# Performance work log

Hardware: AMD Instinct MI355X
Metric: run time of the kernel (lower is better)

## Reference

```python
import jax, jax.numpy as jnp
import numpy as np

B, T, C, H = 16, 2048, 1024, 64  # batch, seq (== block_size), n_embd, head_size


def setup_inputs() -> dict:
    key = jax.random.key(0)
    ks = jax.random.split(key, 4)
    s = 1.0 / np.sqrt(C)  # Linear default init scale
    return {
        "x": jax.random.normal(ks[0], (B, T, C), dtype=jnp.float32),
        "Wq": jax.random.normal(ks[1], (C, H), dtype=jnp.float32) * s,
        "bq": jnp.zeros((H,), dtype=jnp.float32),
        "Wk": jax.random.normal(ks[2], (C, H), dtype=jnp.float32) * s,
        "bk": jnp.zeros((H,), dtype=jnp.float32),
        "Wv": jax.random.normal(ks[3], (C, H), dtype=jnp.float32) * s,
        "bv": jnp.zeros((H,), dtype=jnp.float32),
    }


def reference(x, Wq, bq, Wk, bk, Wv, bv):
    # q, k, v: (B, T, H)
    q = x @ Wq + bq
    k = x @ Wk + bk
    v = x @ Wv + bv
    # scores (B, T, T); NOTE: original code has NO 1/sqrt(H) scaling
    wei = jnp.einsum("btd,bsd->bts", q, k)
    t = x.shape[1]
    causal = jnp.tril(jnp.ones((t, t), dtype=bool))
    wei = jnp.where(causal, wei, -jnp.inf)
    # NOTE: original code applies softmax over dim=1 (query axis), kept faithfully
    wei = jax.nn.softmax(wei, axis=1)
    # dropout is identity at p=0 / eval
    out = jnp.einsum("bts,bsd->btd", wei, v)  # (B, T, H)
    return out
```

## Files before the change

### kernel.cpp

```cpp
#include <hip/hip_runtime.h>
#include <hip/hip_bf16.h>
#include <math.h>

#define TT 2048
#define NB 16

typedef short short8 __attribute__((ext_vector_type(8)));
typedef float f32x4 __attribute__((ext_vector_type(4)));
typedef unsigned short us4 __attribute__((ext_vector_type(4)));

#define MFMA16(a,b,c) __builtin_amdgcn_mfma_f32_16x16x32_bf16((a),(b),(c),0,0,0)

typedef const __attribute__((address_space(1))) unsigned gas_u32;
typedef __attribute__((address_space(3))) unsigned las_u32;

__device__ __forceinline__ void gll16(const void* g, void* l) {
    __builtin_amdgcn_global_load_lds((gas_u32*)g, (las_u32*)l, 16, 0, 0);
}

__device__ __forceinline__ unsigned short bf16rn(float f) {
    unsigned u = __float_as_uint(f);
    u += 0x7FFFu + ((u >> 16) & 1u);
    return (unsigned short)(u >> 16);
}
__device__ __forceinline__ float bf16tof(unsigned short h) {
    return __uint_as_float(((unsigned)h) << 16);
}

__global__ void wprep_kernel(const float* __restrict__ Wq,
                             const float* __restrict__ Wk,
                             const float* __restrict__ Wv,
                             short* __restrict__ WT)
{
    const int m = blockIdx.x >> 6, n = blockIdx.x & 63, tid = threadIdx.x;
    const float* W = (m == 0) ? Wq : ((m == 1) ? Wk : Wv);
    const float sc = (m == 0) ? 1.4426950408889634f : 1.f;
    const int k0 = tid * 4;
    us4 hv, lv;
#pragma unroll
    for (int r = 0; r < 4; ++r) {
        float v = W[(size_t)(k0 + r) * 64 + n] * sc;
        unsigned short hh = bf16rn(v);
        hv[r] = hh;
        lv[r] = bf16rn(v - bf16tof(hh));
    }
    *(us4*)&WT[((size_t)(m * 2 + 0) * 64 + n) * 1024 + k0] = hv;
    *(us4*)&WT[((size_t)(m * 2 + 1) * 64 + n) * 1024 + k0] = lv;
}

__global__ __launch_bounds__(256, 2) void qkv_kernel(
    const float* __restrict__ x,
    const float* __restrict__ bq, const float* __restrict__ bk,
    const float* __restrict__ bv,
    const short* __restrict__ WT,
    short* __restrict__ qhl, short* __restrict__ khl, short* __restrict__ vT)
{
    __shared__ short xs[16384];
    __shared__ short ws[24576];
    const int tid = threadIdx.x;
    const int w = tid >> 6, l15 = tid & 15, g = (tid >> 4) & 3;
    const int t0 = blockIdx.x * 128;

    f32x4 acc[12][2];
    const f32x4 z = {0.f, 0.f, 0.f, 0.f};
#pragma unroll
    for (int i = 0; i < 12; ++i) { acc[i][0] = z; acc[i][1] = z; }

#pragma unroll 1
    for (int kc = 0; kc < 16; ++kc) {
#pragma unroll
        for (int p = 0; p < 12; ++p) {
            int u = tid + p * 256;
            int part = u / 1536; int r = u - part * 1536;
            int kk = r / 768;    int r2 = r - kk * 768;
            int n = r2 >> 2, g8 = r2 & 3;
            int m = n >> 6, nn = n & 63;
            const short* src = WT + (((size_t)((m * 2 + part) * 64 + nn)) << 10)
                                  + kc * 64 + kk * 32 + g8 * 8;
            gll16(src, &ws[((tid & ~63) + p * 256) * 8]);
        }
#pragma unroll
        for (int p = 0; p < 4; ++p) {
            int idx = tid + p * 256;
            int kk = idx >> 9; int rem = idx & 511;
            int row = rem >> 2, g8 = rem & 3;
            const float* xp = x + (size_t)(t0 + row) * 1024 + kc * 64 + kk * 32 + g8 * 8;
            f32x4 a = *(const f32x4*)xp;
            f32x4 b2 = *(const f32x4*)(xp + 4);
            short8 h8, l8;
#pragma unroll
            for (int j = 0; j < 4; ++j) {
                unsigned short hh = bf16rn(a[j]);
                h8[j] = (short)hh; l8[j] = (short)bf16rn(a[j] - bf16tof(hh));
                hh = bf16rn(b2[j]);
                h8[j + 4] = (short)hh; l8[j + 4] = (short)bf16rn(b2[j] - bf16tof(hh));
            }
            *(short8*)&xs[((kk * 128 + row) * 4 + g8) * 8] = h8;
            *(short8*)&xs[(((2 + kk) * 128 + row) * 4 + g8) * 8] = l8;
        }
        __syncthreads();

#pragma unroll
        for (int kk = 0; kk < 2; ++kk) {
            short8 xf[2][2];
#pragma unroll
            for (int m2 = 0; m2 < 2; ++m2)
#pragma unroll
                for (int part = 0; part < 2; ++part)
                    xf[m2][part] = *(const short8*)
                        &xs[(((part * 2 + kk) * 128 + (w * 32 + m2 * 16 + l15)) * 4 + g) * 8];
#pragma unroll
            for (int Nb = 0; Nb < 12; ++Nb) {
                short8 wh = *(const short8*)&ws[(((kk) * 192 + Nb * 16 + l15) * 4 + g) * 8];
                short8 wl = *(const short8*)&ws[(((2 + kk) * 192 + Nb * 16 + l15) * 4 + g) * 8];
#pragma unroll
                for (int m2 = 0; m2 < 2; ++m2) {
                    if (Nb < 8) {
                        acc[Nb][m2] = MFMA16(wh, xf[m2][0], acc[Nb][m2]);
                        acc[Nb][m2] = MFMA16(wh, xf[m2][1], acc[Nb][m2]);
                        acc[Nb][m2] = MFMA16(wl, xf[m2][0], acc[Nb][m2]);
                    } else {
                        acc[Nb][m2] = MFMA16(xf[m2][0], wh, acc[Nb][m2]);
                        acc[Nb][m2] = MFMA16(xf[m2][1], wh, acc[Nb][m2]);
                        acc[Nb][m2] = MFMA16(xf[m2][0], wl, acc[Nb][m2]);
                    }
                }
            }
        }
        __syncthreads();
    }

    const float LOG2E = 1.4426950408889634f;
#pragma unroll
    for (int Nb = 0; Nb < 12; ++Nb) {
#pragma unroll
        for (int m2 = 0; m2 < 2; ++m2) {
            f32x4 a = acc[Nb][m2];
            if (Nb < 8) {
                const bool isq = (Nb < 4);
                const int nbase = (Nb & 3) * 16 + g * 4;
                const int trow = t0 + w * 32 + m2 * 16 + l15;
                const float* bias = isq ? bq : bk;
                us4 hv, lv;
#pragma unroll
                for (int r = 0; r < 4; ++r) {
                    float v = a[r] + (isq ? bias[nbase + r] * LOG2E : bias[nbase + r]);
                    unsigned short hh = bf16rn(v);
                    hv[r] = hh; lv[r] = bf16rn(v - bf16tof(hh));
                }
                short* dst = (isq ? qhl : khl) + ((size_t)trow * 2) * 64 + nbase;
                *(us4*)dst = hv;
                *(us4*)(dst + 64) = lv;
            } else {
                const int d = (Nb - 8) * 16 + l15;
                const int tbase = t0 + w * 32 + m2 * 16 + g * 4;
                const float bvd = bv[d];
                us4 pk;
#pragma unroll
                for (int r = 0; r < 4; ++r) pk[r] = bf16rn(a[r] + bvd);
                const int b = tbase >> 11, ttl = tbase & 2047;
                *(us4*)&vT[((size_t)(b * 64 + d)) * 2048 + ttl] = pk;
            }
        }
    }
}

__global__ __launch_bounds__(256, 2) void colstats_kernel(
    const short* __restrict__ qhl, const short* __restrict__ khl,
    float* __restrict__ ccol)
{
    __shared__ short kb[8192];
    __shared__ short qb[8192];
    const int tid = threadIdx.x;
    const int w = tid >> 6, l15 = tid & 15, g = (tid >> 4) & 3;
    const int sblk = blockIdx.x, b = blockIdx.y;
    const int s0 = sblk * 64;

#pragma unroll
    for (int p = 0; p < 4; ++p) {
        int u = tid + p * 256;
        int part = u >> 9, kk = (u >> 8) & 1, row = (u >> 2) & 63, g8 = u & 3;
        const short* src = khl + ((size_t)(b * TT + s0 + row) * 2 + part) * 64
                               + kk * 32 + g8 * 8;
        gll16(src, &kb[((tid & ~63) + p * 256) * 8]);
    }

    short8 kf[2][2];
    float m_slot[4], d_slot[4];
    const f32x4 z = {0.f, 0.f, 0.f, 0.f};

#pragma unroll 1
    for (int tt = sblk; tt < 32; ++tt) {
#pragma unroll
        for (int p = 0; p < 4; ++p) {
            int u = tid + p * 256;
            int part = u >> 9, kk = (u >> 8) & 1, row = (u >> 2) & 63, g8 = u & 3;
            const short* src = qhl + ((size_t)(b * TT + tt * 64 + row) * 2 + part) * 64
                                   + kk * 32 + g8 * 8;
            gll16(src, &qb[((tid & ~63) + p * 256) * 8]);
        }
        __syncthreads();
        if (tt == sblk) {
#pragma unroll
            for (int kk = 0; kk < 2; ++kk)
#pragma unroll
                for (int part = 0; part < 2; ++part)
                    kf[kk][part] = *(const short8*)
                        &kb[(((part * 2 + kk) * 64 + w * 16 + l15) * 4 + g) * 8];
        }
        f32x4 a4[4];
#pragma unroll
        for (int tb = 0; tb < 4; ++tb) {
            a4[tb] = z;
#pragma unroll
            for (int kk = 0; kk < 2; ++kk) {
                short8 qh = *(const short8*)&qb[(((kk) * 64 + tb * 16 + l15) * 4 + g) * 8];
                short8 ql = *(const short8*)&qb[(((2 + kk) * 64 + tb * 16 + l15) * 4 + g) * 8];
                a4[tb] = MFMA16(kf[kk][0], qh, a4[tb]);
                a4[tb] = MFMA16(kf[kk][0], ql, a4[tb]);
                a4[tb] = MFMA16(kf[kk][1], qh, a4[tb]);
            }
        }
        if (tt == sblk) {
#pragma unroll
            for (int tb = 0; tb < 4; ++tb)
#pragma unroll
                for (int r = 0; r < 4; ++r)
                    if (tb * 16 + l15 < w * 16 + g * 4 + r) a4[tb][r] = -INFINITY;
#pragma unroll
            for (int r = 0; r < 4; ++r) {
                float mx = fmaxf(fmaxf(a4[0][r], a4[1][r]), fmaxf(a4[2][r], a4[3][r]));
                mx = fmaxf(mx, __shfl_xor(mx, 1));
                mx = fmaxf(mx, __shfl_xor(mx, 2));
                mx = fmaxf(mx, __shfl_xor(mx, 4));
                mx = fmaxf(mx, __shfl_xor(mx, 8));
                m_slot[r] = fmaxf(mx, 0.f);
                d_slot[r] = exp2f(a4[0][r] - m_slot[r]) + exp2f(a4[1][r] - m_slot[r])
                          + exp2f(a4[2][r] - m_slot[r]) + exp2f(a4[3][r] - m_slot[r]);
            }
        } else {
#pragma unroll
            for (int r = 0; r < 4; ++r)
                d_slot[r] += exp2f(a4[0][r] - m_slot[r]) + exp2f(a4[1][r] - m_slot[r])
                           + exp2f(a4[2][r] - m_slot[r]) + exp2f(a4[3][r] - m_slot[r]);
        }
        __syncthreads();
    }
#pragma unroll
    for (int r = 0; r < 4; ++r) {
        float dv = d_slot[r];
        dv += __shfl_xor(dv, 1); dv += __shfl_xor(dv, 2);
        dv += __shfl_xor(dv, 4); dv += __shfl_xor(dv, 8);
        d_slot[r] = dv;
    }
    if (l15 == 0) {
        f32x4 c;
#pragma unroll
        for (int r = 0; r < 4; ++r) c[r] = m_slot[r] + log2f(d_slot[r]);
        *(f32x4*)&ccol[(size_t)b * TT + s0 + w * 16 + g * 4] = c;
    }
}

__global__ __launch_bounds__(256, 2) void attnout_kernel(
    const short* __restrict__ qhl, const short* __restrict__ khl,
    const short* __restrict__ vT, const float* __restrict__ ccol,
    float* __restrict__ out)
{
    __shared__ short kb[8192];
    __shared__ short vb[4096];
    __shared__ short eb[4096];
    __shared__ float cb[64];
    const int tid = threadIdx.x;
    const int w = tid >> 6, l15 = tid & 15, g = (tid >> 4) & 3;
    const int tblk = blockIdx.x, b = blockIdx.y;
    const int t0 = tblk * 64;

    short8 qf[4][2][2];
#pragma unroll
    for (int tb = 0; tb < 4; ++tb)
#pragma unroll
        for (int kk = 0; kk < 2; ++kk)
#pragma unroll
            for (int part = 0; part < 2; ++part)
                qf[tb][kk][part] = *(const short8*)
                    (qhl + ((size_t)(b * TT + t0 + tb * 16 + l15) * 2 + part) * 64
                         + kk * 32 + g * 8);

    f32x4 oacc[4];
    const f32x4 z = {0.f, 0.f, 0.f, 0.f};
#pragma unroll
    for (int tb = 0; tb < 4; ++tb) oacc[tb] = z;

#pragma unroll 1
    for (int ss = 0; ss <= tblk; ++ss) {
        const int s0 = ss * 64;
#pragma unroll
        for (int p = 0; p < 4; ++p) {
            int u = tid + p * 256;
            int part = u >> 9, kk = (u >> 8) & 1, row = (u >> 2) & 63, g8 = u & 3;
            gll16(khl + ((size_t)(b * TT + s0 + row) * 2 + part) * 64 + kk * 32 + g8 * 8,
                  &kb[((tid & ~63) + p * 256) * 8]);
        }
#pragma unroll
        for (int p = 0; p < 2; ++p) {
            int u = tid + p * 256;
            int kgs = u >> 8, d = (u >> 2) & 63, g8 = u & 3;
            gll16(vT + ((size_t)(b * 64 + d)) * 2048 + s0 + kgs * 32 + g8 * 8,
                  &vb[((tid & ~63) + p * 256) * 8]);
        }
        if (tid < 64) cb[tid] = ccol[(size_t)b * TT + s0 + tid];
        __syncthreads();

        short8 kf2[2][2];
#pragma unroll
        for (int kk = 0; kk < 2; ++kk)
#pragma unroll
            for (int part = 0; part < 2; ++part)
                kf2[kk][part] = *(const short8*)
                    &kb[(((part * 2 + kk) * 64 + w * 16 + l15) * 4 + g) * 8];

        f32x4 a4[4];
#pragma unroll
        for (int tb = 0; tb < 4; ++tb) {
            a4[tb] = z;
#pragma unroll
            for (int kk = 0; kk < 2; ++kk) {
                a4[tb] = MFMA16(kf2[kk][0], qf[tb][kk][0], a4[tb]);
                a4[tb] = MFMA16(kf2[kk][0], qf[tb][kk][1], a4[tb]);
                a4[tb] = MFMA16(kf2[kk][1], qf[tb][kk][0], a4[tb]);
            }
        }
        const f32x4 c4 = *(const f32x4*)&cb[w * 16 + g * 4];
        const bool diag = (ss == tblk);
#pragma unroll
        for (int tb = 0; tb < 4; ++tb) {
            us4 pk;
#pragma unroll
            for (int r = 0; r < 4; ++r) {
                float e = exp2f(a4[tb][r] - c4[r]);
                if (diag && (tb * 16 + l15 < w * 16 + g * 4 + r)) e = 0.f;
                pk[r] = bf16rn(e);
            }
            const int kgs = w >> 1, g8s = (w & 1) * 2 + (g >> 1), j0 = (g & 1) * 4;
            *(us4*)&eb[((kgs * 64 + tb * 16 + l15) * 4 + g8s) * 8 + j0] = pk;
        }
        __syncthreads();

        short8 vf[2];
#pragma unroll
        for (int kgs = 0; kgs < 2; ++kgs)
            vf[kgs] = *(const short8*)&vb[(((kgs * 64 + w * 16 + l15) * 4 + g) * 8)];
#pragma unroll
        for (int tb = 0; tb < 4; ++tb)
#pragma unroll
            for (int kgs = 0; kgs < 2; ++kgs) {
                short8 ef = *(const short8*)&eb[(((kgs * 64 + tb * 16 + l15) * 4 + g) * 8)];
                oacc[tb] = MFMA16(vf[kgs], ef, oacc[tb]);
            }
        __syncthreads();
    }
#pragma unroll
    for (int tb = 0; tb < 4; ++tb) {
        const int t = t0 + tb * 16 + l15;
        const int d0 = w * 16 + g * 4;
        *(f32x4*)(out + ((size_t)(b * TT + t)) * 64 + d0) = oacc[tb];
    }
}

extern "C" void kernel_launch(void* const* d_in, const int* in_sizes, int n_in,
                              void* d_out, int out_size, void* d_ws, size_t ws_size,
                              hipStream_t stream)
{
    const float* x  = (const float*)d_in[0];
    const float* Wq = (const float*)d_in[1];
    const float* bq = (const float*)d_in[2];
    const float* Wk = (const float*)d_in[3];
    const float* bk = (const float*)d_in[4];
    const float* Wv = (const float*)d_in[5];
    const float* bv = (const float*)d_in[6];

    char* wsb = (char*)d_ws;
    short* qhl = (short*)wsb;
    short* khl = (short*)(wsb + 8388608);
    short* vTb = (short*)(wsb + 16777216);
    short* WT  = (short*)(wsb + 20971520);
    float* ccol = (float*)(wsb + 21757952);

    wprep_kernel<<<dim3(192), 256, 0, stream>>>(Wq, Wk, Wv, WT);
    qkv_kernel<<<dim3(256), 256, 0, stream>>>(x, bq, bk, bv, WT, qhl, khl, vTb);
    colstats_kernel<<<dim3(32, NB), 256, 0, stream>>>(qhl, khl, ccol);
    attnout_kernel<<<dim3(32, NB), 256, 0, stream>>>(qhl, khl, vTb, ccol, (float*)d_out);
}
```

Baseline: 359.4 us.

## Rebalance causal work across blocks and split column-stats with atomic accumulation

The QKV projection now uses 64-row tiles, doubling the grid, and drops the extra low-part MFMA for V. Column stats are split over query chunks with a fixed-zero max and atomically accumulated sums, with a zeroing kernel added before it. The attention-output kernel pairs a short and a long 32-row query tile per block so each block does similar causal work. Dropping the running max risks overflow in exp2 for large scores, atomics make summation order nondeterministic, and computing V in plain bf16 loses some precision.

```diff
diff --git a/kernel.cpp b/kernel.cpp
--- a/kernel.cpp
+++ b/kernel.cpp
@@ -48,6 +48,10 @@
     *(us4*)&WT[((size_t)(m * 2 + 1) * 64 + n) * 1024 + k0] = lv;
 }
 
+__global__ void zero_kernel(float* __restrict__ p) {
+    p[blockIdx.x * 256 + threadIdx.x] = 0.f;
+}
+
 __global__ __launch_bounds__(256, 2) void qkv_kernel(
     const float* __restrict__ x,
     const float* __restrict__ bq, const float* __restrict__ bk,
@@ -55,16 +59,16 @@
     const short* __restrict__ WT,
     short* __restrict__ qhl, short* __restrict__ khl, short* __restrict__ vT)
 {
-    __shared__ short xs[16384];
+    __shared__ short xs[8192];
     __shared__ short ws[24576];
     const int tid = threadIdx.x;
     const int w = tid >> 6, l15 = tid & 15, g = (tid >> 4) & 3;
-    const int t0 = blockIdx.x * 128;
-
-    f32x4 acc[12][2];
+    const int t0 = blockIdx.x * 64;
+
+    f32x4 acc[12];
     const f32x4 z = {0.f, 0.f, 0.f, 0.f};
 #pragma unroll
-    for (int i = 0; i < 12; ++i) { acc[i][0] = z; acc[i][1] = z; }
+    for (int i = 0; i < 12; ++i) acc[i] = z;
 
 #pragma unroll 1
     for (int kc = 0; kc < 16; ++kc) {
@@ -80,9 +84,9 @@
             gll16(src, &ws[((tid & ~63) + p * 256) * 8]);
         }
 #pragma unroll
-        for (int p = 0; p < 4; ++p) {
+        for (int p = 0; p < 2; ++p) {
             int idx = tid + p * 256;
-            int kk = idx >> 9; int rem = idx & 511;
+            int kk = idx >> 8; int rem = idx & 255;
             int row = rem >> 2, g8 = rem & 3;
             const float* xp = x + (size_t)(t0 + row) * 1024 + kc * 64 + kk * 32 + g8 * 8;
             f32x4 a = *(const f32x4*)xp;
@@ -95,35 +99,29 @@
                 hh = bf16rn(b2[j]);
                 h8[j + 4] = (short)hh; l8[j + 4] = (short)bf16rn(b2[j] - bf16tof(hh));
             }
-            *(short8*)&xs[((kk * 128 + row) * 4 + g8) * 8] = h8;
-            *(short8*)&xs[(((2 + kk) * 128 + row) * 4 + g8) * 8] = l8;
+            *(short8*)&xs[((kk * 64 + row) * 4 + g8) * 8] = h8;
+            *(short8*)&xs[(((2 + kk) * 64 + row) * 4 + g8) * 8] = l8;
         }
         __syncthreads();
 
 #pragma unroll
         for (int kk = 0; kk < 2; ++kk) {
-            short8 xf[2][2];
-#pragma unroll
-            for (int m2 = 0; m2 < 2; ++m2)
-#pragma unroll
-                for (int part = 0; part < 2; ++part)
-                    xf[m2][part] = *(const short8*)
-                        &xs[(((part * 2 + kk) * 128 + (w * 32 + m2 * 16 + l15)) * 4 + g) * 8];
+            short8 xf[2];
+#pragma unroll
+            for (int part = 0; part < 2; ++part)
+                xf[part] = *(const short8*)
+                    &xs[(((part * 2 + kk) * 64 + w * 16 + l15) * 4 + g) * 8];
 #pragma unroll
             for (int Nb = 0; Nb < 12; ++Nb) {
-                short8 wh = *(const short8*)&ws[(((kk) * 192 + Nb * 16 + l15) * 4 + g) * 8];
-                short8 wl = *(const short8*)&ws[(((2 + kk) * 192 + Nb * 16 + l15) * 4 + g) * 8];
-#pragma unroll
-                for (int m2 = 0; m2 < 2; ++m2) {
-                    if (Nb < 8) {
-                        acc[Nb][m2] = MFMA16(wh, xf[m2][0], acc[Nb][m2]);
-                        acc[Nb][m2] = MFMA16(wh, xf[m2][1], acc[Nb][m2]);
-                        acc[Nb][m2] = MFMA16(wl, xf[m2][0], acc[Nb][m2]);
-                    } else {
-                        acc[Nb][m2] = MFMA16(xf[m2][0], wh, acc[Nb][m2]);
-                        acc[Nb][m2] = MFMA16(xf[m2][1], wh, acc[Nb][m2]);
-                        acc[Nb][m2] = MFMA16(xf[m2][0], wl, acc[Nb][m2]);
-                    }
+                short8 wh = *(const short8*)&ws[((kk * 192 + Nb * 16 + l15) * 4 + g) * 8];
+                if (Nb < 8) {
+                    short8 wl = *(const short8*)
+                        &ws[(((2 + kk) * 192 + Nb * 16 + l15) * 4 + g) * 8];
+                    acc[Nb] = MFMA16(wh, xf[0], acc[Nb]);
+                    acc[Nb] = MFMA16(wh, xf[1], acc[Nb]);
+                    acc[Nb] = MFMA16(wl, xf[0], acc[Nb]);
+                } else {
+                    acc[Nb] = MFMA16(xf[0], wh, acc[Nb]);
                 }
             }
         }
@@ -133,74 +131,72 @@
     const float LOG2E = 1.4426950408889634f;
 #pragma unroll
     for (int Nb = 0; Nb < 12; ++Nb) {
-#pragma unroll
-        for (int m2 = 0; m2 < 2; ++m2) {
-            f32x4 a = acc[Nb][m2];
-            if (Nb < 8) {
-                const bool isq = (Nb < 4);
-                const int nbase = (Nb & 3) * 16 + g * 4;
-                const int trow = t0 + w * 32 + m2 * 16 + l15;
-                const float* bias = isq ? bq : bk;
-                us4 hv, lv;
-#pragma unroll
-                for (int r = 0; r < 4; ++r) {
-                    float v = a[r] + (isq ? bias[nbase + r] * LOG2E : bias[nbase + r]);
-                    unsigned short hh = bf16rn(v);
-                    hv[r] = hh; lv[r] = bf16rn(v - bf16tof(hh));
-                }
-                short* dst = (isq ? qhl : khl) + ((size_t)trow * 2) * 64 + nbase;
-                *(us4*)dst = hv;
-                *(us4*)(dst + 64) = lv;
-            } else {
-                const int d = (Nb - 8) * 16 + l15;
-                const int tbase = t0 + w * 32 + m2 * 16 + g * 4;
-                const float bvd = bv[d];
-                us4 pk;
-#pragma unroll
-                for (int r = 0; r < 4; ++r) pk[r] = bf16rn(a[r] + bvd);
-                const int b = tbase >> 11, ttl = tbase & 2047;
-                *(us4*)&vT[((size_t)(b * 64 + d)) * 2048 + ttl] = pk;
-            }
-        }
-    }
-}
-
-__global__ __launch_bounds__(256, 2) void colstats_kernel(
+        f32x4 a = acc[Nb];
+        if (Nb < 8) {
+            const bool isq = (Nb < 4);
+            const int nbase = (Nb & 3) * 16 + g * 4;
+            const int trow = t0 + w * 16 + l15;
+            const float* bias = isq ? bq : bk;
+            us4 hv, lv;
+#pragma unroll
+            for (int r = 0; r < 4; ++r) {
+                float v = a[r] + (isq ? bias[nbase + r] * LOG2E : bias[nbase + r]);
+                unsigned short hh = bf16rn(v);
+                hv[r] = hh; lv[r] = bf16rn(v - bf16tof(hh));
+            }
+            short* dst = (isq ? qhl : khl) + ((size_t)trow * 2) * 64 + nbase;
+            *(us4*)dst = hv;
+            *(us4*)(dst + 64) = lv;
+        } else {
+            const int d = (Nb - 8) * 16 + l15;
+            const int tbase = t0 + w * 16 + g * 4;
+            const float bvd = bv[d];
+            us4 pk;
+#pragma unroll
+            for (int r = 0; r < 4; ++r) pk[r] = bf16rn(a[r] + bvd);
+            const int b = tbase >> 11, ttl = tbase & 2047;
+            *(us4*)&vT[((size_t)(b * 64 + d)) * 2048 + ttl] = pk;
+        }
+    }
+}
+
+__global__ __launch_bounds__(256, 4) void colstats_kernel(
     const short* __restrict__ qhl, const short* __restrict__ khl,
-    float* __restrict__ ccol)
+    float* __restrict__ dcol)
 {
     __shared__ short kb[8192];
     __shared__ short qb[8192];
     const int tid = threadIdx.x;
     const int w = tid >> 6, l15 = tid & 15, g = (tid >> 4) & 3;
-    const int sblk = blockIdx.x, b = blockIdx.y;
+    const int sblk = blockIdx.x, tc = blockIdx.y, b = blockIdx.z;
+    const int tt0 = max(sblk, tc * 8), tt1 = min(32, tc * 8 + 8);
+    if (tt0 >= tt1) return;
     const int s0 = sblk * 64;
+    const int sl = w * 16 + g * 4;
 
 #pragma unroll
     for (int p = 0; p < 4; ++p) {
         int u = tid + p * 256;
         int part = u >> 9, kk = (u >> 8) & 1, row = (u >> 2) & 63, g8 = u & 3;
-        const short* src = khl + ((size_t)(b * TT + s0 + row) * 2 + part) * 64
-                               + kk * 32 + g8 * 8;
-        gll16(src, &kb[((tid & ~63) + p * 256) * 8]);
+        gll16(khl + ((size_t)(b * TT + s0 + row) * 2 + part) * 64 + kk * 32 + g8 * 8,
+              &kb[((tid & ~63) + p * 256) * 8]);
     }
 
     short8 kf[2][2];
-    float m_slot[4], d_slot[4];
+    float dsl[4] = {0.f, 0.f, 0.f, 0.f};
     const f32x4 z = {0.f, 0.f, 0.f, 0.f};
 
 #pragma unroll 1
-    for (int tt = sblk; tt < 32; ++tt) {
+    for (int tt = tt0; tt < tt1; ++tt) {
 #pragma unroll
         for (int p = 0; p < 4; ++p) {
             int u = tid + p * 256;
             int part = u >> 9, kk = (u >> 8) & 1, row = (u >> 2) & 63, g8 = u & 3;
-            const short* src = qhl + ((size_t)(b * TT + tt * 64 + row) * 2 + part) * 64
-                                   + kk * 32 + g8 * 8;
-            gll16(src, &qb[((tid & ~63) + p * 256) * 8]);
-        }
-        __syncthreads();
-        if (tt == sblk) {
+            gll16(qhl + ((size_t)(b * TT + tt * 64 + row) * 2 + part) * 64 + kk * 32 + g8 * 8,
+                  &qb[((tid & ~63) + p * 256) * 8]);
+        }
+        __syncthreads();
+        if (tt == tt0) {
 #pragma unroll
             for (int kk = 0; kk < 2; ++kk)
 #pragma unroll
@@ -208,162 +204,178 @@
                     kf[kk][part] = *(const short8*)
                         &kb[(((part * 2 + kk) * 64 + w * 16 + l15) * 4 + g) * 8];
         }
-        f32x4 a4[4];
 #pragma unroll
         for (int tb = 0; tb < 4; ++tb) {
-            a4[tb] = z;
+            f32x4 a = z;
 #pragma unroll
             for (int kk = 0; kk < 2; ++kk) {
-                short8 qh = *(const short8*)&qb[(((kk) * 64 + tb * 16 + l15) * 4 + g) * 8];
+                short8 qh = *(const short8*)&qb[((kk * 64 + tb * 16 + l15) * 4 + g) * 8];
                 short8 ql = *(const short8*)&qb[(((2 + kk) * 64 + tb * 16 + l15) * 4 + g) * 8];
-                a4[tb] = MFMA16(kf[kk][0], qh, a4[tb]);
-                a4[tb] = MFMA16(kf[kk][0], ql, a4[tb]);
-                a4[tb] = MFMA16(kf[kk][1], qh, a4[tb]);
-            }
-        }
-        if (tt == sblk) {
-#pragma unroll
-            for (int tb = 0; tb < 4; ++tb)
+                a = MFMA16(kf[kk][0], qh, a);
+                a = MFMA16(kf[kk][0], ql, a);
+                a = MFMA16(kf[kk][1], qh, a);
+            }
+            if (tt == sblk) {
 #pragma unroll
                 for (int r = 0; r < 4; ++r)
-                    if (tb * 16 + l15 < w * 16 + g * 4 + r) a4[tb][r] = -INFINITY;
-#pragma unroll
-            for (int r = 0; r < 4; ++r) {
-                float mx = fmaxf(fmaxf(a4[0][r], a4[1][r]), fmaxf(a4[2][r], a4[3][r]));
-                mx = fmaxf(mx, __shfl_xor(mx, 1));
-                mx = fmaxf(mx, __shfl_xor(mx, 2));
-                mx = fmaxf(mx, __shfl_xor(mx, 4));
-                mx = fmaxf(mx, __shfl_xor(mx, 8));
-                m_slot[r] = fmaxf(mx, 0.f);
-                d_slot[r] = exp2f(a4[0][r] - m_slot[r]) + exp2f(a4[1][r] - m_slot[r])
-                          + exp2f(a4[2][r] - m_slot[r]) + exp2f(a4[3][r] - m_slot[r]);
-            }
-        } else {
-#pragma unroll
-            for (int r = 0; r < 4; ++r)
-                d_slot[r] += exp2f(a4[0][r] - m_slot[r]) + exp2f(a4[1][r] - m_slot[r])
-                           + exp2f(a4[2][r] - m_slot[r]) + exp2f(a4[3][r] - m_slot[r]);
+                    if (tb * 16 + l15 < sl + r) a[r] = -INFINITY;
+            }
+#pragma unroll
+            for (int r = 0; r < 4; ++r) dsl[r] += exp2f(a[r]);
         }
         __syncthreads();
     }
 #pragma unroll
     for (int r = 0; r < 4; ++r) {
-        float dv = d_slot[r];
+        float dv = dsl[r];
         dv += __shfl_xor(dv, 1); dv += __shfl_xor(dv, 2);
         dv += __shfl_xor(dv, 4); dv += __shfl_xor(dv, 8);
-        d_slot[r] = dv;
+        dsl[r] = dv;
     }
     if (l15 == 0) {
-        f32x4 c;
-#pragma unroll
-        for (int r = 0; r < 4; ++r) c[r] = m_slot[r] + log2f(d_slot[r]);
-        *(f32x4*)&ccol[(size_t)b * TT + s0 + w * 16 + g * 4] = c;
+#pragma unroll
+        for (int r = 0; r < 4; ++r)
+            atomicAdd(&dcol[(size_t)b * TT + s0 + sl + r], dsl[r]);
     }
 }
 
 __global__ __launch_bounds__(256, 2) void attnout_kernel(
     const short* __restrict__ qhl, const short* __restrict__ khl,
-    const short* __restrict__ vT, const float* __restrict__ ccol,
+    const short* __restrict__ vT, const float* __restrict__ dcol,
     float* __restrict__ out)
 {
     __shared__ short kb[8192];
     __shared__ short vb[4096];
-    __shared__ short eb[4096];
+    __shared__ short ebA[2048];
+    __shared__ short ebB[2048];
     __shared__ float cb[64];
     const int tid = threadIdx.x;
     const int w = tid >> 6, l15 = tid & 15, g = (tid >> 4) & 3;
-    const int tblk = blockIdx.x, b = blockIdx.y;
-    const int t0 = tblk * 64;
-
-    short8 qf[4][2][2];
-#pragma unroll
-    for (int tb = 0; tb < 4; ++tb)
+    const int p = blockIdx.x, b = blockIdx.y;
+    const int iA = p, iB = 63 - p;
+    const int nA = iA >> 1, nB = iB >> 1;
+    const int sl = w * 16 + g * 4;
+
+    short8 qfA[2][2][2], qfB[2][2][2];
+#pragma unroll
+    for (int tb = 0; tb < 2; ++tb)
 #pragma unroll
         for (int kk = 0; kk < 2; ++kk)
 #pragma unroll
-            for (int part = 0; part < 2; ++part)
-                qf[tb][kk][part] = *(const short8*)
-                    (qhl + ((size_t)(b * TT + t0 + tb * 16 + l15) * 2 + part) * 64
+            for (int part = 0; part < 2; ++part) {
+                qfA[tb][kk][part] = *(const short8*)
+                    (qhl + ((size_t)(b * TT + iA * 32 + tb * 16 + l15) * 2 + part) * 64
                          + kk * 32 + g * 8);
-
-    f32x4 oacc[4];
+                qfB[tb][kk][part] = *(const short8*)
+                    (qhl + ((size_t)(b * TT + iB * 32 + tb * 16 + l15) * 2 + part) * 64
+                         + kk * 32 + g * 8);
+            }
+
+    f32x4 oaccA[2], oaccB[2];
     const f32x4 z = {0.f, 0.f, 0.f, 0.f};
-#pragma unroll
-    for (int tb = 0; tb < 4; ++tb) oacc[tb] = z;
+    oaccA[0] = z; oaccA[1] = z; oaccB[0] = z; oaccB[1] = z;
 
 #pragma unroll 1
-    for (int ss = 0; ss <= tblk; ++ss) {
+    for (int ss = 0; ss <= nB; ++ss) {
         const int s0 = ss * 64;
 #pragma unroll
-        for (int p = 0; p < 4; ++p) {
-            int u = tid + p * 256;
+        for (int pp = 0; pp < 4; ++pp) {
+            int u = tid + pp * 256;
             int part = u >> 9, kk = (u >> 8) & 1, row = (u >> 2) & 63, g8 = u & 3;
             gll16(khl + ((size_t)(b * TT + s0 + row) * 2 + part) * 64 + kk * 32 + g8 * 8,
-                  &kb[((tid & ~63) + p * 256) * 8]);
-        }
-#pragma unroll
-        for (int p = 0; p < 2; ++p) {
-            int u = tid + p * 256;
+                  &kb[((tid & ~63) + pp * 256) * 8]);
+        }
+#pragma unroll
+        for (int pp = 0; pp < 2; ++pp) {
+            int u = tid + pp * 256;
             int kgs = u >> 8, d = (u >> 2) & 63, g8 = u & 3;
             gll16(vT + ((size_t)(b * 64 + d)) * 2048 + s0 + kgs * 32 + g8 * 8,
-                  &vb[((tid & ~63) + p * 256) * 8]);
-        }
-        if (tid < 64) cb[tid] = ccol[(size_t)b * TT + s0 + tid];
-        __syncthreads();
-
-        short8 kf2[2][2];
+                  &vb[((tid & ~63) + pp * 256) * 8]);
+        }
+        if (tid < 64) cb[tid] = log2f(dcol[(size_t)b * TT + s0 + tid]);
+        __syncthreads();
+
+        short8 kf[2][2];
 #pragma unroll
         for (int kk = 0; kk < 2; ++kk)
 #pragma unroll
             for (int part = 0; part < 2; ++part)
-                kf2[kk][part] = *(const short8*)
+                kf[kk][part] = *(const short8*)
                     &kb[(((part * 2 + kk) * 64 + w * 16 + l15) * 4 + g) * 8];
 
-        f32x4 a4[4];
-#pragma unroll
-        for (int tb = 0; tb < 4; ++tb) {
-            a4[tb] = z;
+        const f32x4 c4 = *(const f32x4*)&cb[sl];
+        const bool actA = (ss <= nA);
+        const int kgs = w >> 1, g8s = (w & 1) * 2 + (g >> 1), j0 = (g & 1) * 4;
+
+#pragma unroll
+        for (int tb = 0; tb < 2; ++tb) {
+            f32x4 a = z;
 #pragma unroll
             for (int kk = 0; kk < 2; ++kk) {
-                a4[tb] = MFMA16(kf2[kk][0], qf[tb][kk][0], a4[tb]);
-                a4[tb] = MFMA16(kf2[kk][0], qf[tb][kk][1], a4[tb]);
-                a4[tb] = MFMA16(kf2[kk][1], qf[tb][kk][0], a4[tb]);
-            }
-        }
-        const f32x4 c4 = *(const f32x4*)&cb[w * 16 + g * 4];
-        const bool diag = (ss == tblk);
-#pragma unroll
-        for (int tb = 0; tb < 4; ++tb) {
+                a = MFMA16(kf[kk][0], qfB[tb][kk][0], a);
+                a = MFMA16(kf[kk][0], qfB[tb][kk][1], a);
+                a = MFMA16(kf[kk][1], qfB[tb][kk][0], a);
+            }
+            const int tg = iB * 32 + tb * 16 + l15;
             us4 pk;
 #pragma unroll
             for (int r = 0; r < 4; ++r) {
-                float e = exp2f(a4[tb][r] - c4[r]);
-                if (diag && (tb * 16 + l15 < w * 16 + g * 4 + r)) e = 0.f;
+                float e = (s0 + sl + r <= tg) ? exp2f(a[r] - c4[r]) : 0.f;
                 pk[r] = bf16rn(e);
             }
-            const int kgs = w >> 1, g8s = (w & 1) * 2 + (g >> 1), j0 = (g & 1) * 4;
-            *(us4*)&eb[((kgs * 64 + tb * 16 + l15) * 4 + g8s) * 8 + j0] = pk;
+            *(us4*)&ebB[((kgs * 32 + tb * 16 + l15) * 4 + g8s) * 8 + j0] = pk;
+        }
+        if (actA) {
+#pragma unroll
+            for (int tb = 0; tb < 2; ++tb) {
+                f32x4 a = z;
+#pragma unroll
+                for (int kk = 0; kk < 2; ++kk) {
+                    a = MFMA16(kf[kk][0], qfA[tb][kk][0], a);
+                    a = MFMA16(kf[kk][0], qfA[tb][kk][1], a);
+                    a = MFMA16(kf[kk][1], qfA[tb][kk][0], a);
+                }
+                const int tg = iA * 32 + tb * 16 + l15;
+                us4 pk;
+#pragma unroll
+                for (int r = 0; r < 4; ++r) {
+                    float e = (s0 + sl + r <= tg) ? exp2f(a[r] - c4[r]) : 0.f;
+                    pk[r] = bf16rn(e);
+                }
+                *(us4*)&ebA[((kgs * 32 + tb * 16 + l15) * 4 + g8s) * 8 + j0] = pk;
+            }
         }
         __syncthreads();
 
         short8 vf[2];
 #pragma unroll
-        for (int kgs = 0; kgs < 2; ++kgs)
-            vf[kgs] = *(const short8*)&vb[(((kgs * 64 + w * 16 + l15) * 4 + g) * 8)];
-#pragma unroll
-        for (int tb = 0; tb < 4; ++tb)
-#pragma unroll
-            for (int kgs = 0; kgs < 2; ++kgs) {
-                short8 ef = *(const short8*)&eb[(((kgs * 64 + tb * 16 + l15) * 4 + g) * 8)];
-                oacc[tb] = MFMA16(vf[kgs], ef, oacc[tb]);
-            }
-        __syncthreads();
-    }
-#pragma unroll
-    for (int tb = 0; tb < 4; ++tb) {
-        const int t = t0 + tb * 16 + l15;
-        const int d0 = w * 16 + g * 4;
-        *(f32x4*)(out + ((size_t)(b * TT + t)) * 64 + d0) = oacc[tb];
+        for (int kg = 0; kg < 2; ++kg)
+            vf[kg] = *(const short8*)&vb[((kg * 64 + w * 16 + l15) * 4 + g) * 8];
+#pragma unroll
+        for (int tb = 0; tb < 2; ++tb)
+#pragma unroll
+            for (int kg = 0; kg < 2; ++kg) {
+                short8 ef = *(const short8*)&ebB[((kg * 32 + tb * 16 + l15) * 4 + g) * 8];
+                oaccB[tb] = MFMA16(vf[kg], ef, oaccB[tb]);
+            }
+        if (actA) {
+#pragma unroll
+            for (int tb = 0; tb < 2; ++tb)
+#pragma unroll
+                for (int kg = 0; kg < 2; ++kg) {
+                    short8 ef = *(const short8*)&ebA[((kg * 32 + tb * 16 + l15) * 4 + g) * 8];
+                    oaccA[tb] = MFMA16(vf[kg], ef, oaccA[tb]);
+                }
+        }
+        __syncthreads();
+    }
+
+#pragma unroll
+    for (int tb = 0; tb < 2; ++tb) {
+        const int tA = iA * 32 + tb * 16 + l15;
+        const int tB = iB * 32 + tb * 16 + l15;
+        *(f32x4*)(out + ((size_t)(b * TT + tA)) * 64 + sl) = oaccA[tb];
+        *(f32x4*)(out + ((size_t)(b * TT + tB)) * 64 + sl) = oaccB[tb];
     }
 }
 
@@ -384,10 +396,11 @@
     short* khl = (short*)(wsb + 8388608);
     short* vTb = (short*)(wsb + 16777216);
     short* WT  = (short*)(wsb + 20971520);
-    float* ccol = (float*)(wsb + 21757952);
-
+    float* dcol = (float*)(wsb + 21757952);
+
+    zero_kernel<<<dim3(128), 256, 0, stream>>>(dcol);
     wprep_kernel<<<dim3(192), 256, 0, stream>>>(Wq, Wk, Wv, WT);
-    qkv_kernel<<<dim3(256), 256, 0, stream>>>(x, bq, bk, bv, WT, qhl, khl, vTb);
-    colstats_kernel<<<dim3(32, NB), 256, 0, stream>>>(qhl, khl, ccol);
-    attnout_kernel<<<dim3(32, NB), 256, 0, stream>>>(qhl, khl, vTb, ccol, (float*)d_out);
-}
+    qkv_kernel<<<dim3(512), 256, 0, stream>>>(x, bq, bk, bv, WT, qhl, khl, vTb);
+    colstats_kernel<<<dim3(32, 4, NB), 256, 0, stream>>>(qhl, khl, dcol);
+    attnout_kernel<<<dim3(32, NB), 256, 0, stream>>>(qhl, khl, vTb, dcol, (float*)d_out);
+}
```

Result: faster. 310.3 us (-13.7%).
